# Kernel tuning notes

Measured on AMD Instinct MI355X. Metric: run time of the kernel, lower is better.

Reference implementation:

```python
import jax, jax.numpy as jnp
import numpy as np

B, N, D, H, L = 2, 1024, 256, 4, 18
HD = D // H  # 64 per-head dim
SINKHORN_ITERS = 100
EPS = 1e-6


def _ln(x, g, b):
    # repo's custom LayerNorm: normalize over channel dim (-2) of [B,C,N], torch.std is unbiased (ddof=1)
    mean = jnp.mean(x, axis=1, keepdims=True)
    std = jnp.std(x, axis=1, keepdims=True, ddof=1)
    return g[None, :, None] * (x - mean) / (std + EPS) + b[None, :, None]


def _conv(w, b, x):
    # Conv1d kernel_size=1 on [B,Cin,N] == pointwise linear
    return jnp.einsum('oi,bin->bon', w, x) + b[None, :, None]


def setup_inputs() -> dict:
    key = jax.random.key(0)
    ks = iter(jax.random.split(key, 64))
    def nrm(shape, scale=1.0):
        return jax.random.normal(next(ks), shape, dtype=jnp.float32) * scale
    inp = {}
    inp['desc0'] = nrm((B, D, N))
    inp['desc1'] = nrm((B, D, N))
    inp['kpts0'] = jax.random.uniform(next(ks), (B, N, 2), dtype=jnp.float32)
    inp['kpts1'] = jax.random.uniform(next(ks), (B, N, 2), dtype=jnp.float32)
    inp['scores0'] = jax.random.uniform(next(ks), (B, N), dtype=jnp.float32)
    inp['scores1'] = jax.random.uniform(next(ks), (B, N), dtype=jnp.float32)
    ch = [3, 32, 64, 128, 256]
    for i in range(4):
        ci, co = ch[i], ch[i + 1]
        inp['kenc_w%d' % i] = nrm((co, ci), 1.0 / np.sqrt(ci))
        inp['kenc_b%d' % i] = jnp.zeros((co,), jnp.float32)
        if i < 3:
            inp['kenc_g%d' % i] = jnp.ones((co,), jnp.float32)
            inp['kenc_be%d' % i] = jnp.zeros((co,), jnp.float32)
    s = 1.0 / np.sqrt(D)
    for nm in ['q', 'k', 'v', 'm']:
        inp['gnn_%sw' % nm] = nrm((L, D, D), s)
        inp['gnn_%sb' % nm] = jnp.zeros((L, D), jnp.float32)
    inp['gnn_w1'] = nrm((L, 2 * D, 2 * D), 1.0 / np.sqrt(2 * D))
    inp['gnn_b1'] = jnp.zeros((L, 2 * D), jnp.float32)
    inp['gnn_g1'] = jnp.ones((L, 2 * D), jnp.float32)
    inp['gnn_be1'] = jnp.zeros((L, 2 * D), jnp.float32)
    inp['gnn_w2'] = nrm((L, D, 2 * D), 1.0 / np.sqrt(2 * D))
    inp['gnn_b2'] = jnp.zeros((L, D), jnp.float32)
    inp['final_w'] = nrm((D, D), s)
    inp['final_b'] = jnp.zeros((D,), jnp.float32)
    return inp


def reference(desc0, desc1, kpts0, kpts1, scores0, scores1, kenc_w0, kenc_b0, kenc_g0, kenc_be0, kenc_w1, kenc_b1, kenc_g1, kenc_be1, kenc_w2, kenc_b2, kenc_g2, kenc_be2, kenc_w3, kenc_b3, gnn_qw, gnn_qb, gnn_kw, gnn_kb, gnn_vw, gnn_vb, gnn_mw, gnn_mb, gnn_w1, gnn_b1, gnn_g1, gnn_be1, gnn_w2, gnn_b2, final_w, final_b):
    def kenc(kpts, sc):
        x = jnp.concatenate([jnp.transpose(kpts, (0, 2, 1)), sc[:, None, :]], axis=1)  # [B,3,N]
        x = jax.nn.relu(_ln(_conv(kenc_w0, kenc_b0, x), kenc_g0, kenc_be0))
        x = jax.nn.relu(_ln(_conv(kenc_w1, kenc_b1, x), kenc_g1, kenc_be1))
        x = jax.nn.relu(_ln(_conv(kenc_w2, kenc_b2, x), kenc_g2, kenc_be2))
        return _conv(kenc_w3, kenc_b3, x)

    d0 = desc0 + kenc(kpts0, scores0)
    d1 = desc1 + kenc(kpts1, scores1)

    def gnn_layer(i, x, src):
        b = x.shape[0]
        q = _conv(gnn_qw[i], gnn_qb[i], x).reshape(b, HD, H, -1)
        k = _conv(gnn_kw[i], gnn_kb[i], src).reshape(b, HD, H, -1)
        v = _conv(gnn_vw[i], gnn_vb[i], src).reshape(b, HD, H, -1)
        sc = jnp.einsum('bdhn,bdhm->bhnm', q, k) / np.sqrt(HD).astype(np.float32)
        prob = jax.nn.softmax(sc, axis=-1)
        msg = jnp.einsum('bhnm,bdhm->bdhn', prob, v).reshape(b, D, -1)
        msg = _conv(gnn_mw[i], gnn_mb[i], msg)
        y = jnp.concatenate([x, msg], axis=1)  # [B,2D,N]
        y = jax.nn.relu(_ln(_conv(gnn_w1[i], gnn_b1[i], y), gnn_g1[i], gnn_be1[i]))
        return _conv(gnn_w2[i], gnn_b2[i], y)

    for i in range(L):  # names alternate self(even)/cross(odd)
        if i % 2 == 1:
            s0, s1 = d1, d0
        else:
            s0, s1 = d0, d1
        d0n = d0 + gnn_layer(i, d0, s0)
        d1n = d1 + gnn_layer(i, d1, s1)
        d0, d1 = d0n, d1n

    m0 = _conv(final_w, final_b, d0)
    m1 = _conv(final_w, final_b, d1)
    sc = jnp.einsum('bdn,bdm->bnm', m0, m1) / np.sqrt(D).astype(np.float32)

    # log-domain Sinkhorn with uniform marginals log_mu = log_nu = -log(m+n)
    n = sc.shape[1]
    norm = -jnp.log(jnp.asarray(2.0 * n, dtype=sc.dtype))
    u0 = jnp.zeros(sc.shape[:2], sc.dtype)
    v0 = jnp.zeros(sc.shape[:2], sc.dtype)

    def body(_, uv):
        u, v = uv
        u = norm - jax.scipy.special.logsumexp(sc + v[:, None, :], axis=2)
        v = norm - jax.scipy.special.logsumexp(sc + u[:, :, None], axis=1)
        return (u, v)

    u, v = jax.lax.fori_loop(0, SINKHORN_ITERS, body, (u0, v0))
    Z = sc + u[:, :, None] + v[:, None, :] - norm
    return Z
```

## Files before the change

### kernel.cpp

```cpp
#include <hip/hip_runtime.h>


#define NPOS 1024
#define DIM  256
#define NLAYER 18

static constexpr float NORMC = -7.6246189861593985f;

typedef float f32x4 __attribute__((ext_vector_type(4)));
typedef unsigned int u32x2 __attribute__((ext_vector_type(2)));
typedef unsigned int u32x4 __attribute__((ext_vector_type(4)));

__device__ __forceinline__ float wredmax(float v){
#pragma unroll
  for (int o = 32; o > 0; o >>= 1) v = fmaxf(v, __shfl_xor(v, o));
  return v;
}
__device__ __forceinline__ float wredsum(float v){
#pragma unroll
  for (int o = 32; o > 0; o >>= 1) v += __shfl_xor(v, o);
  return v;
}

__device__ __forceinline__ void cvt2(float x, unsigned short& h, unsigned short& l){
  unsigned xb = __float_as_uint(x);
  h = (unsigned short)(xb >> 16);
  float r = x - __uint_as_float(xb & 0xFFFF0000u);
  l = (unsigned short)(__float_as_uint(r) >> 16);
}
__device__ __forceinline__ u32x2 pack4(const unsigned short* s){
  u32x2 p;
  p.x = (unsigned)s[0] | ((unsigned)s[1] << 16);
  p.y = (unsigned)s[2] | ((unsigned)s[3] << 16);
  return p;
}
__device__ __forceinline__ void mfma_bf16(f32x4& acc, const u32x4& a, const u32x4& b){
  asm volatile("v_mfma_f32_16x16x32_bf16 %0, %1, %2, %0" : "+v"(acc) : "v"(a), "v"(b));
}
__device__ __forceinline__ void mfma_bf16_hz(f32x4& acc, const u32x4& a, const u32x4& b){
  asm volatile("s_nop 3\n\tv_mfma_f32_16x16x32_bf16 %0, %1, %2, %0" : "+v"(acc) : "v"(a), "v"(b));
}
#define MFMA_FENCE() asm volatile("s_nop 7\n\ts_nop 7\n\ts_nop 7" :::)


template<bool RESID, bool SPLIT>
__device__ __forceinline__ void gemm_mfma_core(
    const float* __restrict__ W, const float* __restrict__ bias,
    const float* __restrict__ Xb, const float* __restrict__ X2b,
    float* __restrict__ Ob, const float* __restrict__ Rb,
    int K, int o0, int n0)
{
  __shared__ unsigned short lwh[4096], lwl[4096];
  __shared__ unsigned short lxh[4096], lxl[4096];
  const int t = threadIdx.x;
  const int lane = t & 63, w = t >> 6;
  f32x4 acc[4];
#pragma unroll
  for (int i = 0; i < 4; i++) acc[i] = (f32x4)0.f;

  const int so = t & 63, skq = (t >> 6) << 4;
  const int sn = t & 63, skg = t >> 6;
  const int wmi = so >> 4, wol = so & 15;
  const int wks = skq >> 5, whalf = (skq >> 4) & 1;
  const int xni = sn >> 4, xnl = sn & 15;
  const int xks = skg >> 1, xhalf = skg & 1;

  float4 pw[4];
  float px[16];
  const float* wbase = W + (long)(o0 + so) * K + skq;
  auto loadchunk = [&](int kp) {
#pragma unroll
    for (int q = 0; q < 4; q++) pw[q] = *(const float4*)(wbase + kp + q * 4);
    const float* xr = (SPLIT && kp >= 256) ? (X2b + (long)(kp - 256) * NPOS)
                                           : (Xb + (long)kp * NPOS);
#pragma unroll
    for (int q = 0; q < 4; q++)
#pragma unroll
      for (int j = 0; j < 4; j++)
        px[q * 4 + j] = xr[(long)(skg * 16 + q * 4 + j) * NPOS + n0 + sn];
  };

  loadchunk(0);
  for (int kp = 0; kp < K; kp += 64) {
#pragma unroll
    for (int q = 0; q < 4; q++) {
      unsigned short h[4], l[4];
      cvt2(pw[q].x, h[0], l[0]); cvt2(pw[q].y, h[1], l[1]);
      cvt2(pw[q].z, h[2], l[2]); cvt2(pw[q].w, h[3], l[3]);
      int idx = ((wmi * 2 + wks) * 64 + wol + 16 * q) * 8 + whalf * 4;
      *(u32x2*)&lwh[idx] = pack4(h);
      *(u32x2*)&lwl[idx] = pack4(l);
    }
#pragma unroll
    for (int q = 0; q < 4; q++) {
      unsigned short h[4], l[4];
#pragma unroll
      for (int j = 0; j < 4; j++) cvt2(px[q * 4 + j], h[j], l[j]);
      int idx = ((xni * 2 + xks) * 64 + xnl + 16 * q) * 8 + xhalf * 4;
      *(u32x2*)&lxh[idx] = pack4(h);
      *(u32x2*)&lxl[idx] = pack4(l);
    }
    __syncthreads();
    if (kp + 64 < K) loadchunk(kp + 64);
#pragma unroll
    for (int ks = 0; ks < 2; ks++) {
      u32x4 Bh = *(const u32x4*)&lxh[((w * 2 + ks) * 64 + lane) * 8];
      u32x4 Bl = *(const u32x4*)&lxl[((w * 2 + ks) * 64 + lane) * 8];
#pragma unroll
      for (int mi = 0; mi < 4; mi++) {
        u32x4 Ah = *(const u32x4*)&lwh[((mi * 2 + ks) * 64 + lane) * 8];
        u32x4 Al = *(const u32x4*)&lwl[((mi * 2 + ks) * 64 + lane) * 8];
        mfma_bf16(acc[mi], Ah, Bh);
        mfma_bf16(acc[mi], Ah, Bl);
        mfma_bf16(acc[mi], Al, Bh);
      }
    }
    __syncthreads();
  }
  MFMA_FENCE();
  const int l15 = lane & 15, l4 = lane >> 4;
  const int n = n0 + (w << 4) + l15;
#pragma unroll
  for (int mi = 0; mi < 4; mi++) {
#pragma unroll
    for (int r = 0; r < 4; r++) {
      int o = o0 + mi * 16 + l4 * 4 + r;
      float val = acc[mi][r] + bias[o];
      if (RESID) val += Rb[(long)o * NPOS + n];
      Ob[(long)o * NPOS + n] = val;
    }
  }
}

template<bool RESID, bool SPLIT>
__global__ __launch_bounds__(256, 4) void gemm_mfma(
    const float* __restrict__ W, const float* __restrict__ bias,
    const float* __restrict__ X, const float* __restrict__ X2,
    float* __restrict__ out, const float* __restrict__ R,
    int K, long xbs, long x2bs, long obs, long rbs)
{
  const int bz = blockIdx.z;
  gemm_mfma_core<RESID, SPLIT>(W, bias,
      X + (long)bz * xbs, SPLIT ? (X2 + (long)bz * x2bs) : X,
      out + (long)bz * obs, RESID ? (R + (long)bz * rbs) : out,
      K, blockIdx.y * 64, blockIdx.x * 64);
}

__global__ __launch_bounds__(256, 4) void gemm_qkv_mfma(
    const float* __restrict__ Wq, const float* __restrict__ Bq,
    const float* __restrict__ Wk, const float* __restrict__ Bk,
    const float* __restrict__ Wv, const float* __restrict__ Bv,
    const float* __restrict__ X, float* __restrict__ out)
{
  const int z = blockIdx.z;
  const int which = z >> 2, bz = z & 3;
  const float* W    = (which == 0) ? Wq : (which == 1) ? Wk : Wv;
  const float* bias = (which == 0) ? Bq : (which == 1) ? Bk : Bv;
  gemm_mfma_core<false, false>(W, bias,
      X + (long)bz * (DIM * NPOS), nullptr,
      out + (long)which * 1048576 + (long)bz * (DIM * NPOS), nullptr,
      256, blockIdx.y * 64, blockIdx.x * 64);
}

__global__ __launch_bounds__(256, 4) void gemm_w1s_mfma(
    const float* __restrict__ W, const float* __restrict__ bias,
    const float* __restrict__ X, const float* __restrict__ X2,
    float* __restrict__ out, float* __restrict__ psum, float* __restrict__ psq)
{
  __shared__ unsigned short lwh[4096], lwl[4096];
  __shared__ unsigned short lxh[4096], lxl[4096];
  const int t = threadIdx.x;
  const int lane = t & 63, w = t >> 6;
  const int bz = blockIdx.z, o0 = blockIdx.y * 64, n0 = blockIdx.x * 64;
  const float* Xb  = X  + (long)bz * (DIM * NPOS);
  const float* X2b = X2 + (long)bz * (DIM * NPOS);
  float* Ob = out + (long)bz * (2L * DIM * NPOS);
  f32x4 acc[4];
#pragma unroll
  for (int i = 0; i < 4; i++) acc[i] = (f32x4)0.f;

  const int so = t & 63, skq = (t >> 6) << 4;
  const int sn = t & 63, skg = t >> 6;
  const int wmi = so >> 4, wol = so & 15;
  const int wks = skq >> 5, whalf = (skq >> 4) & 1;
  const int xni = sn >> 4, xnl = sn & 15;
  const int xks = skg >> 1, xhalf = skg & 1;

  float4 pw[4];
  float px[16];
  const float* wbase = W + (long)(o0 + so) * 512 + skq;
  auto loadchunk = [&](int kp) {
#pragma unroll
    for (int q = 0; q < 4; q++) pw[q] = *(const float4*)(wbase + kp + q * 4);
    const float* xr = (kp >= 256) ? (X2b + (long)(kp - 256) * NPOS)
                                  : (Xb + (long)kp * NPOS);
#pragma unroll
    for (int q = 0; q < 4; q++)
#pragma unroll
      for (int j = 0; j < 4; j++)
        px[q * 4 + j] = xr[(long)(skg * 16 + q * 4 + j) * NPOS + n0 + sn];
  };

  loadchunk(0);
  for (int kp = 0; kp < 512; kp += 64) {
#pragma unroll
    for (int q = 0; q < 4; q++) {
      unsigned short h[4], l[4];
      cvt2(pw[q].x, h[0], l[0]); cvt2(pw[q].y, h[1], l[1]);
      cvt2(pw[q].z, h[2], l[2]); cvt2(pw[q].w, h[3], l[3]);
      int idx = ((wmi * 2 + wks) * 64 + wol + 16 * q) * 8 + whalf * 4;
      *(u32x2*)&lwh[idx] = pack4(h);
      *(u32x2*)&lwl[idx] = pack4(l);
    }
#pragma unroll
    for (int q = 0; q < 4; q++) {
      unsigned short h[4], l[4];
#pragma unroll
      for (int j = 0; j < 4; j++) cvt2(px[q * 4 + j], h[j], l[j]);
      int idx = ((xni * 2 + xks) * 64 + xnl + 16 * q) * 8 + xhalf * 4;
      *(u32x2*)&lxh[idx] = pack4(h);
      *(u32x2*)&lxl[idx] = pack4(l);
    }
    __syncthreads();
    if (kp + 64 < 512) loadchunk(kp + 64);
#pragma unroll
    for (int ks = 0; ks < 2; ks++) {
      u32x4 Bh = *(const u32x4*)&lxh[((w * 2 + ks) * 64 + lane) * 8];
      u32x4 Bl = *(const u32x4*)&lxl[((w * 2 + ks) * 64 + lane) * 8];
#pragma unroll
      for (int mi = 0; mi < 4; mi++) {
        u32x4 Ah = *(const u32x4*)&lwh[((mi * 2 + ks) * 64 + lane) * 8];
        u32x4 Al = *(const u32x4*)&lwl[((mi * 2 + ks) * 64 + lane) * 8];
        mfma_bf16(acc[mi], Ah, Bh);
        mfma_bf16(acc[mi], Ah, Bl);
        mfma_bf16(acc[mi], Al, Bh);
      }
    }
    __syncthreads();
  }
  MFMA_FENCE();
  const int l15 = lane & 15, l4 = lane >> 4;
  const int n = n0 + (w << 4) + l15;
  float ps = 0.f, pq = 0.f;
#pragma unroll
  for (int mi = 0; mi < 4; mi++) {
#pragma unroll
    for (int r = 0; r < 4; r++) {
      int o = o0 + mi * 16 + l4 * 4 + r;
      float val = acc[mi][r] + bias[o];
      Ob[(long)o * NPOS + n] = val;
      ps += val; pq += val * val;
    }
  }
  ps += __shfl_xor(ps, 16); ps += __shfl_xor(ps, 32);
  pq += __shfl_xor(pq, 16); pq += __shfl_xor(pq, 32);
  if (l4 == 0) {
    long sidx = ((long)blockIdx.y * 4 + bz) * NPOS + n;
    psum[sidx] = ps;
    psq[sidx]  = pq;
  }
}

__global__ __launch_bounds__(256, 4) void gemm_w2ln_mfma(
    const float* __restrict__ W, const float* __restrict__ bias,
    const float* __restrict__ X, const float* __restrict__ ga, const float* __restrict__ be,
    const float* __restrict__ psum, const float* __restrict__ psq,
    float* __restrict__ out, const float* __restrict__ R)
{
  __shared__ unsigned short lwh[4096], lwl[4096];
  __shared__ unsigned short lxh[4096], lxl[4096];
  __shared__ float meanv[64], invv[64];
  const int t = threadIdx.x;
  const int lane = t & 63, w = t >> 6;
  const int bz = blockIdx.z, o0 = blockIdx.y * 64, n0 = blockIdx.x * 64;
  const float* Xb = X + (long)bz * (2L * DIM * NPOS);
  float* Ob = out + (long)bz * (DIM * NPOS);
  const float* Rb = R + (long)bz * (DIM * NPOS);
  if (t < 64) {
    int n = n0 + t;
    float S = 0.f, S2 = 0.f;
#pragma unroll
    for (int j = 0; j < 8; j++) {
      long sidx = ((long)j * 4 + bz) * NPOS + n;
      S += psum[sidx]; S2 += psq[sidx];
    }
    float mean = S * (1.f / 512.f);
    float var  = (S2 - 512.f * mean * mean) * (1.f / 511.f);
    meanv[t] = mean;
    invv[t]  = 1.f / (sqrtf(fmaxf(var, 0.f)) + 1e-6f);
  }
  __syncthreads();

  f32x4 acc[4];
#pragma unroll
  for (int i = 0; i < 4; i++) acc[i] = (f32x4)0.f;

  const int so = t & 63, skq = (t >> 6) << 4;
  const int sn = t & 63, skg = t >> 6;
  const int wmi = so >> 4, wol = so & 15;
  const int wks = skq >> 5, whalf = (skq >> 4) & 1;
  const int xni = sn >> 4, xnl = sn & 15;
  const int xks = skg >> 1, xhalf = skg & 1;
  const float mn = meanv[sn], iv = invv[sn];

  float4 pw[4];
  float px[16];
  const float* wbase = W + (long)(o0 + so) * 512 + skq;
  auto loadchunk = [&](int kp) {
#pragma unroll
    for (int q = 0; q < 4; q++) pw[q] = *(const float4*)(wbase + kp + q * 4);
#pragma unroll
    for (int q = 0; q < 4; q++)
#pragma unroll
      for (int j = 0; j < 4; j++)
        px[q * 4 + j] = Xb[(long)(kp + skg * 16 + q * 4 + j) * NPOS + n0 + sn];
  };

  loadchunk(0);
  for (int kp = 0; kp < 512; kp += 64) {
#pragma unroll
    for (int q = 0; q < 4; q++) {
      unsigned short h[4], l[4];
      cvt2(pw[q].x, h[0], l[0]); cvt2(pw[q].y, h[1], l[1]);
      cvt2(pw[q].z, h[2], l[2]); cvt2(pw[q].w, h[3], l[3]);
      int idx = ((wmi * 2 + wks) * 64 + wol + 16 * q) * 8 + whalf * 4;
      *(u32x2*)&lwh[idx] = pack4(h);
      *(u32x2*)&lwl[idx] = pack4(l);
    }
#pragma unroll
    for (int q = 0; q < 4; q++) {
      unsigned short h[4], l[4];
#pragma unroll
      for (int j = 0; j < 4; j++) {
        int cc = kp + skg * 16 + q * 4 + j;
        float x = fmaxf((px[q * 4 + j] - mn) * iv * ga[cc] + be[cc], 0.f);
        cvt2(x, h[j], l[j]);
      }
      int idx = ((xni * 2 + xks) * 64 + xnl + 16 * q) * 8 + xhalf * 4;
      *(u32x2*)&lxh[idx] = pack4(h);
      *(u32x2*)&lxl[idx] = pack4(l);
    }
    __syncthreads();
    if (kp + 64 < 512) loadchunk(kp + 64);
#pragma unroll
    for (int ks = 0; ks < 2; ks++) {
      u32x4 Bh = *(const u32x4*)&lxh[((w * 2 + ks) * 64 + lane) * 8];
      u32x4 Bl = *(const u32x4*)&lxl[((w * 2 + ks) * 64 + lane) * 8];
#pragma unroll
      for (int mi = 0; mi < 4; mi++) {
        u32x4 Ah = *(const u32x4*)&lwh[((mi * 2 + ks) * 64 + lane) * 8];
        u32x4 Al = *(const u32x4*)&lwl[((mi * 2 + ks) * 64 + lane) * 8];
        mfma_bf16(acc[mi], Ah, Bh);
        mfma_bf16(acc[mi], Ah, Bl);
        mfma_bf16(acc[mi], Al, Bh);
      }
    }
    __syncthreads();
  }
  MFMA_FENCE();
  const int l15 = lane & 15, l4 = lane >> 4;
  const int n = n0 + (w << 4) + l15;
#pragma unroll
  for (int mi = 0; mi < 4; mi++) {
#pragma unroll
    for (int r = 0; r < 4; r++) {
      int o = o0 + mi * 16 + l4 * 4 + r;
      Ob[(long)o * NPOS + n] = acc[mi][r] + bias[o] + Rb[(long)o * NPOS + n];
    }
  }
}

__global__ __launch_bounds__(256) void scores_mfma(
    const float* __restrict__ Mm, float* __restrict__ S0, float* __restrict__ S1, float scale)
{
  __shared__ unsigned short lah[4096], lal[4096];
  __shared__ unsigned short lbh[8192], lbl[8192];
  const int t = threadIdx.x, lane = t & 63, w = t >> 6;
  const int m0 = blockIdx.x * 128, n0 = blockIdx.y * 64;
  const int g = blockIdx.z & 1, dir = blockIdx.z >> 1;
  const long BS2 = 2L * DIM * NPOS;
  const float* Ag = (dir ? (Mm + BS2) : Mm) + (long)g * DIM * NPOS;
  const float* Bg = (dir ? Mm : (Mm + BS2)) + (long)g * DIM * NPOS;
  float* Sg = (dir ? S1 : S0) + (long)g * NPOS * NPOS;
  f32x4 acc[4][2];
#pragma unroll
  for (int i = 0; i < 4; i++)
#pragma unroll
    for (int j = 0; j < 2; j++) acc[i][j] = (f32x4)0.f;

  const int an = t & 63, acq = t >> 6;
  const int bm = t & 127, bkg = t >> 7;
  const int ami = an >> 4, anl = an & 15;
  const int aks = acq >> 1, ahalf = acq & 1;
  const int bni = bm >> 4, bnl = bm & 15;

  for (int cp = 0; cp < 256; cp += 64) {
#pragma unroll
    for (int q = 0; q < 4; q++) {
      unsigned short h[4], l[4];
#pragma unroll
      for (int j = 0; j < 4; j++) {
        float x = Ag[(long)(cp + acq * 16 + q * 4 + j) * NPOS + n0 + an];
        cvt2(x, h[j], l[j]);
      }
      int idx = ((ami * 2 + aks) * 64 + anl + 16 * q) * 8 + ahalf * 4;
      *(u32x2*)&lah[idx] = pack4(h);
      *(u32x2*)&lal[idx] = pack4(l);
    }
#pragma unroll
    for (int q = 0; q < 8; q++) {
      unsigned short h[4], l[4];
#pragma unroll
      for (int j = 0; j < 4; j++) {
        float x = Bg[(long)(cp + bkg * 32 + q * 4 + j) * NPOS + m0 + bm];
        cvt2(x, h[j], l[j]);
      }
      int qm = q & 3, half = (q >> 2) & 1;
      int idx = ((bni * 2 + bkg) * 64 + bnl + 16 * qm) * 8 + half * 4;
      *(u32x2*)&lbh[idx] = pack4(h);
      *(u32x2*)&lbl[idx] = pack4(l);
    }
    __syncthreads();
#pragma unroll
    for (int ks = 0; ks < 2; ks++) {
      u32x4 Ah[4], Al[4], Bh[2], Bl[2];
#pragma unroll
      for (int mi = 0; mi < 4; mi++) {
        Ah[mi] = *(const u32x4*)&lah[((mi * 2 + ks) * 64 + lane) * 8];
        Al[mi] = *(const u32x4*)&lal[((mi * 2 + ks) * 64 + lane) * 8];
      }
#pragma unroll
      for (int ni = 0; ni < 2; ni++) {
        int gg = w * 2 + ni;
        Bh[ni] = *(const u32x4*)&lbh[((gg * 2 + ks) * 64 + lane) * 8];
        Bl[ni] = *(const u32x4*)&lbl[((gg * 2 + ks) * 64 + lane) * 8];
      }
#pragma unroll
      for (int mi = 0; mi < 4; mi++)
#pragma unroll
        for (int ni = 0; ni < 2; ni++) {
          mfma_bf16(acc[mi][ni], Ah[mi], Bh[ni]);
          mfma_bf16(acc[mi][ni], Ah[mi], Bl[ni]);
          mfma_bf16(acc[mi][ni], Al[mi], Bh[ni]);
        }
    }
    __syncthreads();
  }
  MFMA_FENCE();
  const int l15 = lane & 15, l4 = lane >> 4;
#pragma unroll
  for (int mi = 0; mi < 4; mi++)
#pragma unroll
    for (int r = 0; r < 4; r++) {
      int n = n0 + mi * 16 + l4 * 4 + r;
#pragma unroll
      for (int ni = 0; ni < 2; ni++) {
        int m = m0 + (w * 2 + ni) * 16 + l15;
        Sg[(long)n * NPOS + m] = acc[mi][ni][r] * scale;
      }
    }
}

__global__ __launch_bounds__(256) void flash_mfma(
    const float* __restrict__ Q, const float* __restrict__ K,
    const float* __restrict__ V, float* __restrict__ O, int cross)
{
  __shared__ unsigned short lqh[4096], lql[4096];
  __shared__ unsigned short lkh[4096], lkl[4096];
  __shared__ unsigned short lvh[4096], lvl[4096];
  const int t = threadIdx.x, lane = t & 63, w = t >> 6;
  const int lin = blockIdx.x + 16 * blockIdx.y;
  const int xcd = lin & 7, slot = lin >> 3;
  const int g = xcd * 2 + (slot >> 4);
  const int n0 = (slot & 15) * 64;
  const int s = g >> 3, b = (g >> 2) & 1, h = g & 3;
  const int sba = s * 2 + b;
  const int sbb = (cross ? (1 - s) : s) * 2 + b;
  const float* Qg = Q + ((long)sba * DIM + h) * NPOS;
  const float* Kg = K + ((long)sbb * DIM + h) * NPOS;
  const float* Vg = V + ((long)sbb * DIM + h) * NPOS;
  float*       Og = O + ((long)sba * DIM + h) * NPOS;

  {
    const int n = t & 63;
#pragma unroll
    for (int qq = 0; qq < 4; qq++) {
      int dq = (t >> 6) + qq * 4;
      unsigned short hh[4], ll[4];
#pragma unroll
      for (int j = 0; j < 4; j++) {
        float x = Qg[(long)(4 * (dq * 4 + j)) * NPOS + n0 + n] * 0.125f;
        cvt2(x, hh[j], ll[j]);
      }
      int idx = (((n >> 4) * 2 + (dq >> 3)) * 64 + (n & 15) + 16 * (dq & 3)) * 8 + ((dq >> 2) & 1) * 4;
      *(u32x2*)&lqh[idx] = pack4(hh);
      *(u32x2*)&lql[idx] = pack4(ll);
    }
  }

  float M = -1e30f, L = 0.f;
  f32x4 acc_o[4];
#pragma unroll
  for (int i = 0; i < 4; i++) acc_o[i] = (f32x4)0.f;

  const int km = t & 63;
  const int vmq = t & 15;
  float pk[16];
  float4 pv4[4];
  auto loadKV = [&](int m0) {
#pragma unroll
    for (int qq = 0; qq < 4; qq++) {
      int dq = (t >> 6) + qq * 4;
#pragma unroll
      for (int j = 0; j < 4; j++)
        pk[qq * 4 + j] = Kg[(long)(4 * (dq * 4 + j)) * NPOS + m0 + km];
    }
#pragma unroll
    for (int pp = 0; pp < 4; pp++) {
      int d = (t >> 4) + pp * 16;
      pv4[pp] = *(const float4*)(Vg + (long)(4 * d) * NPOS + m0 + vmq * 4);
    }
  };

  loadKV(0);
  for (int mt = 0; mt < 16; mt++) {
    __syncthreads();
#pragma unroll
    for (int qq = 0; qq < 4; qq++) {
      int dq = (t >> 6) + qq * 4;
      unsigned short hh[4], ll[4];
#pragma unroll
      for (int j = 0; j < 4; j++) cvt2(pk[qq * 4 + j], hh[j], ll[j]);
      int idx = (((km >> 4) * 2 + (dq >> 3)) * 64 + (km & 15) + 16 * (dq & 3)) * 8 + ((dq >> 2) & 1) * 4;
      *(u32x2*)&lkh[idx] = pack4(hh);
      *(u32x2*)&lkl[idx] = pack4(ll);
    }
#pragma unroll
    for (int pp = 0; pp < 4; pp++) {
      int d = (t >> 4) + pp * 16;
      unsigned short hh[4], ll[4];
      cvt2(pv4[pp].x, hh[0], ll[0]); cvt2(pv4[pp].y, hh[1], ll[1]);
      cvt2(pv4[pp].z, hh[2], ll[2]); cvt2(pv4[pp].w, hh[3], ll[3]);
      int idx = (((d >> 4) * 2 + (vmq >> 3)) * 64 + (d & 15) + 16 * (vmq & 3)) * 8 + ((vmq >> 2) & 1) * 4;
      *(u32x2*)&lvh[idx] = pack4(hh);
      *(u32x2*)&lvl[idx] = pack4(ll);
    }
    __syncthreads();
    if (mt + 1 < 16) loadKV((mt + 1) * 64);

    f32x4 s_[4];
#pragma unroll
    for (int ms = 0; ms < 4; ms++) s_[ms] = (f32x4)0.f;
#pragma unroll
    for (int ks = 0; ks < 2; ks++) {
      u32x4 Bh = *(const u32x4*)&lqh[((w * 2 + ks) * 64 + lane) * 8];
      u32x4 Bl = *(const u32x4*)&lql[((w * 2 + ks) * 64 + lane) * 8];
#pragma unroll
      for (int ms = 0; ms < 4; ms++) {
        u32x4 Ah = *(const u32x4*)&lkh[((ms * 2 + ks) * 64 + lane) * 8];
        u32x4 Al = *(const u32x4*)&lkl[((ms * 2 + ks) * 64 + lane) * 8];
        mfma_bf16_hz(s_[ms], Ah, Bh);
        mfma_bf16_hz(s_[ms], Ah, Bl);
        mfma_bf16_hz(s_[ms], Al, Bh);
      }
    }
    MFMA_FENCE();

    float p[4][4];
    float tm = -1e30f;
#pragma unroll
    for (int ms = 0; ms < 4; ms++)
#pragma unroll
      for (int r = 0; r < 4; r++) tm = fmaxf(tm, s_[ms][r]);
    tm = fmaxf(tm, __shfl_xor(tm, 16));
    tm = fmaxf(tm, __shfl_xor(tm, 32));
    float nm = fmaxf(M, tm);
    float fi = __expf(M - nm);
    float rs = 0.f;
#pragma unroll
    for (int ms = 0; ms < 4; ms++)
#pragma unroll
      for (int r = 0; r < 4; r++) {
        float pv = __expf(s_[ms][r] - nm);
        p[ms][r] = pv; rs += pv;
      }
    rs += __shfl_xor(rs, 16);
    rs += __shfl_xor(rs, 32);
    L = L * fi + rs;
    M = nm;

    u32x4 Bp_h[2], Bp_l[2];
#pragma unroll
    for (int ks = 0; ks < 2; ks++) {
      unsigned short h0[4], l0[4], h1[4], l1[4];
#pragma unroll
      for (int r = 0; r < 4; r++) {
        cvt2(p[2 * ks][r], h0[r], l0[r]);
        cvt2(p[2 * ks + 1][r], h1[r], l1[r]);
      }
      u32x2 a = pack4(h0), bq = pack4(h1);
      Bp_h[ks].x = a.x; Bp_h[ks].y = a.y; Bp_h[ks].z = bq.x; Bp_h[ks].w = bq.y;
      u32x2 c = pack4(l0), dq = pack4(l1);
      Bp_l[ks].x = c.x; Bp_l[ks].y = c.y; Bp_l[ks].z = dq.x; Bp_l[ks].w = dq.y;
    }
#pragma unroll
    for (int ds = 0; ds < 4; ds++)
#pragma unroll
      for (int r = 0; r < 4; r++) acc_o[ds][r] *= fi;

#pragma unroll
    for (int ks = 0; ks < 2; ks++)
#pragma unroll
      for (int ds = 0; ds < 4; ds++) {
        u32x4 Ah = *(const u32x4*)&lvh[((ds * 2 + ks) * 64 + lane) * 8];
        u32x4 Al = *(const u32x4*)&lvl[((ds * 2 + ks) * 64 + lane) * 8];
        mfma_bf16_hz(acc_o[ds], Ah, Bp_h[ks]);
        mfma_bf16_hz(acc_o[ds], Ah, Bp_l[ks]);
        mfma_bf16_hz(acc_o[ds], Al, Bp_h[ks]);
      }
    MFMA_FENCE();
  }

  MFMA_FENCE();
  float linv = 1.f / L;
  const int nn = n0 + (w << 4) + (lane & 15);
#pragma unroll
  for (int ds = 0; ds < 4; ds++)
#pragma unroll
    for (int r = 0; r < 4; r++) {
      int d = ds * 16 + (lane >> 4) * 4 + r;
      Og[(long)(4 * d) * NPOS + nn] = acc_o[ds][r] * linv;
    }
}

__global__ __launch_bounds__(256) void foldW1(
    const float* __restrict__ w1g, const float* __restrict__ mwg,
    const float* __restrict__ b1g, const float* __restrict__ mbg,
    float* __restrict__ Wcat, float* __restrict__ bcat)
{
  const int z = blockIdx.z;
  const float* W1 = w1g + (long)z * 262144;
  const float* Wm = mwg + (long)z * 65536;
  float* out = Wcat + (long)z * 262144;
  const int o0 = blockIdx.y * 64;
  const int t = threadIdx.x;
  if (blockIdx.x >= 4) {
    const int c0 = (int)(blockIdx.x - 4) * 64;
    const int row = t >> 2, cb = (t & 3) * 16;
#pragma unroll
    for (int q = 0; q < 4; q++) {
      *(float4*)(out + (long)(o0 + row) * 512 + c0 + cb + 4 * q) =
          *(const float4*)(W1 + (long)(o0 + row) * 512 + c0 + cb + 4 * q);
    }
    if (blockIdx.x == 4 && t < 64) {
      int o = o0 + t;
      float acc = b1g[z * 512 + o];
      const float* wr = W1 + (long)o * 512 + 256;
      const float* bm = mbg + z * 256;
      for (int j = 0; j < 256; j++) acc += wr[j] * bm[j];
      bcat[z * 512 + o] = acc;
    }
    return;
  }
  __shared__ float As[16][64], Xs[16][64];
  const int c0 = blockIdx.x * 64;
  const int lr = t >> 2, lc = (t & 3) << 2;
  const int xr = t >> 4, xc = (t & 15) << 2;
  const int ty = t >> 4, tx = t & 15;
  float acc[4][4] = {};
  for (int j0 = 0; j0 < 256; j0 += 16) {
    float4 av = *(const float4*)(W1 + (long)(o0 + lr) * 512 + 256 + j0 + lc);
    As[lc + 0][lr] = av.x; As[lc + 1][lr] = av.y; As[lc + 2][lr] = av.z; As[lc + 3][lr] = av.w;
    *(float4*)&Xs[xr][xc] = *(const float4*)(Wm + (long)(j0 + xr) * 256 + c0 + xc);
    __syncthreads();
#pragma unroll
    for (int kk = 0; kk < 16; kk++) {
      float4 a4 = *(const float4*)&As[kk][ty << 2];
      float4 b4 = *(const float4*)&Xs[kk][tx << 2];
      acc[0][0] += a4.x * b4.x; acc[0][1] += a4.x * b4.y; acc[0][2] += a4.x * b4.z; acc[0][3] += a4.x * b4.w;
      acc[1][0] += a4.y * b4.x; acc[1][1] += a4.y * b4.y; acc[1][2] += a4.y * b4.z; acc[1][3] += a4.y * b4.w;
      acc[2][0] += a4.z * b4.x; acc[2][1] += a4.z * b4.y; acc[2][2] += a4.z * b4.z; acc[2][3] += a4.z * b4.w;
      acc[3][0] += a4.w * b4.x; acc[3][1] += a4.w * b4.y; acc[3][2] += a4.w * b4.z; acc[3][3] += a4.w * b4.w;
    }
    __syncthreads();
  }
#pragma unroll
  for (int i = 0; i < 4; i++) {
    float4 v = make_float4(acc[i][0], acc[i][1], acc[i][2], acc[i][3]);
    *(float4*)(out + (long)(o0 + (ty << 2) + i) * 512 + 256 + c0 + (tx << 2)) = v;
  }
}

__global__ __launch_bounds__(256) void sinkK(const float* __restrict__ S,
                                             const float* __restrict__ vin,
                                             float* __restrict__ uout, float norm)
{
  const int r = blockIdx.x * 4 + (threadIdx.x >> 6);
  const int lane = threadIdx.x & 63;
  const int b = r >> 10;
  const float* row = S + (long)r * NPOS;
  const float* vv = vin + (b << 10);
  float vals[16]; float mx = -1e30f;
#pragma unroll
  for (int i = 0; i < 16; i++) { vals[i] = row[lane + i * 64] + vv[lane + i * 64]; mx = fmaxf(mx, vals[i]); }
  mx = wredmax(mx);
  float s = 0.f;
#pragma unroll
  for (int i = 0; i < 16; i++) s += __expf(vals[i] - mx);
  s = wredsum(s);
  if (lane == 0) uout[r] = norm - (mx + __logf(s));
}

__global__ __launch_bounds__(256) void finZ(float* __restrict__ Z, const float* __restrict__ u,
                                            const float* __restrict__ v, float norm)
{
  long i = (long)blockIdx.x * 256 + threadIdx.x;
  float4 z = ((float4*)Z)[i];
  long e = i << 2;
  int b = (int)(e >> 20); int n = (int)((e >> 10) & 1023); int m = (int)(e & 1023);
  float add = u[(b << 10) + n] - norm;
  const float* vb = v + (b << 10) + m;
  z.x += add + vb[0]; z.y += add + vb[1]; z.z += add + vb[2]; z.w += add + vb[3];
  ((float4*)Z)[i] = z;
}

template<int O, int I>
__device__ __forceinline__ void stage_mm(const float* __restrict__ W, const float* __restrict__ bias,
                                         const float* xin, float* xout, int g, int p)
{
  for (int o = g; o < O; o += 4) {
    float acc = bias[o];
    const float* wr = W + o * I;
    for (int i = 0; i < I; i++) acc += wr[i] * xin[i * 64 + p];
    xout[o * 64 + p] = acc;
  }
  __syncthreads();
}
template<int C>
__device__ __forceinline__ void stage_ln(float* x, const float* __restrict__ ga,
                                         const float* __restrict__ be, float* red, int g, int p)
{
  float s = 0.f, s2 = 0.f;
  for (int c = g; c < C; c += 4) { float v = x[c * 64 + p]; s += v; s2 += v * v; }
  red[g * 64 + p] = s; red[(4 + g) * 64 + p] = s2;
  __syncthreads();
  float S  = red[p] + red[64 + p] + red[128 + p] + red[192 + p];
  float S2 = red[256 + p] + red[320 + p] + red[384 + p] + red[448 + p];
  float mean = S / (float)C;
  float var  = (S2 - (float)C * mean * mean) / (float)(C - 1);
  float inv  = 1.f / (sqrtf(fmaxf(var, 0.f)) + 1e-6f);
  __syncthreads();
  for (int c = g; c < C; c += 4) {
    float v = (x[c * 64 + p] - mean) * inv * ga[c] + be[c];
    x[c * 64 + p] = fmaxf(v, 0.f);
  }
  __syncthreads();
}

__global__ __launch_bounds__(256) void kencK(
    const float* __restrict__ kpts0, const float* __restrict__ scr0, const float* __restrict__ desc0,
    const float* __restrict__ kpts1, const float* __restrict__ scr1, const float* __restrict__ desc1,
    const float* __restrict__ w0, const float* __restrict__ b0, const float* __restrict__ g0, const float* __restrict__ be0,
    const float* __restrict__ w1, const float* __restrict__ b1, const float* __restrict__ g1, const float* __restrict__ be1,
    const float* __restrict__ w2, const float* __restrict__ b2, const float* __restrict__ g2, const float* __restrict__ be2,
    const float* __restrict__ w3, const float* __restrict__ b3,
    float* __restrict__ dout)
{
  __shared__ float a0[3 * 64], a1[32 * 64], a2[64 * 64], a3[128 * 64], red[8 * 64];
  const int t = threadIdx.x, p = t & 63, g = t >> 6;
  const int strm = blockIdx.x >> 5;
  const int blk = blockIdx.x & 31;
  const float* kpts = strm ? kpts1 : kpts0;
  const float* scr  = strm ? scr1  : scr0;
  const float* desc = strm ? desc1 : desc0;
  float* dst = dout + (long)strm * 2 * DIM * NPOS;
  const int b = blk >> 4, n0 = (blk & 15) << 6;
  if (g == 0)      a0[p]        = kpts[((b << 10) + n0 + p) * 2];
  else if (g == 1) a0[64 + p]   = kpts[((b << 10) + n0 + p) * 2 + 1];
  else if (g == 2) a0[128 + p]  = scr[(b << 10) + n0 + p];
  __syncthreads();
  stage_mm<32, 3>(w0, b0, a0, a1, g, p);   stage_ln<32>(a1, g0, be0, red, g, p);
  stage_mm<64, 32>(w1, b1, a1, a2, g, p);  stage_ln<64>(a2, g1, be1, red, g, p);
  stage_mm<128, 64>(w2, b2, a2, a3, g, p); stage_ln<128>(a3, g2, be2, red, g, p);
  for (int o = g; o < 256; o += 4) {
    float acc = b3[o];
    const float* wr = w3 + o * 128;
    for (int i = 0; i < 128; i++) acc += wr[i] * a3[i * 64 + p];
    long idx = ((long)(b * 256 + o) << 10) + n0 + p;
    dst[idx] = desc[idx] + acc;
  }
}

extern "C" void kernel_launch(void* const* d_in, const int* in_sizes, int n_in,
                              void* d_out, int out_size, void* d_ws, size_t ws_size,
                              hipStream_t stream)
{
  (void)in_sizes; (void)n_in; (void)out_size; (void)ws_size;
  const float* desc0   = (const float*)d_in[0];
  const float* desc1   = (const float*)d_in[1];
  const float* kpts0   = (const float*)d_in[2];
  const float* kpts1   = (const float*)d_in[3];
  const float* scores0 = (const float*)d_in[4];
  const float* scores1 = (const float*)d_in[5];
  const float* kw0 = (const float*)d_in[6],  *kb0 = (const float*)d_in[7],
             * kg0 = (const float*)d_in[8],  *kbe0 = (const float*)d_in[9];
  const float* kw1 = (const float*)d_in[10], *kb1 = (const float*)d_in[11],
             * kg1 = (const float*)d_in[12], *kbe1 = (const float*)d_in[13];
  const float* kw2 = (const float*)d_in[14], *kb2 = (const float*)d_in[15],
             * kg2 = (const float*)d_in[16], *kbe2 = (const float*)d_in[17];
  const float* kw3 = (const float*)d_in[18], *kb3 = (const float*)d_in[19];
  const float* qw = (const float*)d_in[20], *qbi = (const float*)d_in[21];
  const float* kw = (const float*)d_in[22], *kbi = (const float*)d_in[23];
  const float* vw = (const float*)d_in[24], *vbi = (const float*)d_in[25];
  const float* mw = (const float*)d_in[26], *mbi = (const float*)d_in[27];
  const float* w1g = (const float*)d_in[28], *b1g = (const float*)d_in[29];
  const float* g1g = (const float*)d_in[30], *be1g = (const float*)d_in[31];
  const float* w2g = (const float*)d_in[32], *b2g = (const float*)d_in[33];
  const float* fw = (const float*)d_in[34], *fb = (const float*)d_in[35];

  float* ws = (float*)d_ws;
  const long M1 = 1048576;
  float* d_a  = ws;
  float* d_b  = ws + 1 * M1;
  float* qb   = ws + 2 * M1;
  float* kb   = ws + 3 * M1;
  float* vb   = ws + 4 * M1;
  float* msgb = ws + 5 * M1;
  float* Pb   = ws + 8 * M1;
  float* t1   = Pb;
  float* Wcat = ws + 10 * M1;
  float* bcat = ws + 15 * M1;
  float* psum = ws + 15 * M1 + 16384;
  float* psq  = psum + 32768;
  float* uu   = ws + 16 * M1;
  float* vv   = uu + 2048;
  float* scT  = qb;
  float* mmb  = msgb;

  foldW1<<<dim3(8, 8, 18), 256, 0, stream>>>(w1g, mw, b1g, mbi, Wcat, bcat);

  kencK<<<64, 256, 0, stream>>>(kpts0, scores0, desc0, kpts1, scores1, desc1,
      kw0, kb0, kg0, kbe0, kw1, kb1, kg1, kbe1, kw2, kb2, kg2, kbe2, kw3, kb3, d_a);

  float* dc = d_a; float* dn = d_b;
  const long BS1 = (long)DIM * NPOS;
  for (int i = 0; i < NLAYER; i++) {
    int cross = i & 1;
    const float* Wq = qw + (long)i * 65536;  const float* Bq = qbi + (long)i * 256;
    const float* Wk = kw + (long)i * 65536;  const float* Bk = kbi + (long)i * 256;
    const float* Wv = vw + (long)i * 65536;  const float* Bv = vbi + (long)i * 256;
    const float* W1 = Wcat + (long)i * 262144; const float* B1 = bcat + (long)i * 512;
    const float* G1 = g1g + (long)i * 512;    const float* BE1 = be1g + (long)i * 512;
    const float* W2 = w2g + (long)i * 131072; const float* B2 = b2g + (long)i * 256;

    gemm_qkv_mfma<<<dim3(16, 4, 12), 256, 0, stream>>>(Wq, Bq, Wk, Bk, Wv, Bv, dc, qb);
    flash_mfma<<<dim3(16, 16), 256, 0, stream>>>(qb, kb, vb, msgb, cross);
    gemm_w1s_mfma<<<dim3(16, 8, 4), 256, 0, stream>>>(W1, B1, dc, msgb, t1, psum, psq);
    gemm_w2ln_mfma<<<dim3(16, 4, 4), 256, 0, stream>>>(W2, B2, t1, G1, BE1, psum, psq, dn, dc);
    float* tmp = dc; dc = dn; dn = tmp;
  }

  gemm_mfma<false, false><<<dim3(16, 4, 4), 256, 0, stream>>>(
      fw, fb, dc, nullptr, mmb, nullptr, 256, BS1, 0, BS1, 0);
  float* scf = (float*)d_out;
  scores_mfma<<<dim3(8, 16, 4), 256, 0, stream>>>(mmb, scf, scT, 0.0625f);

  hipMemsetAsync(vv, 0, 2048 * sizeof(float), stream);
  for (int it = 0; it < 100; it++) {
    sinkK<<<512, 256, 0, stream>>>(scf, vv, uu, NORMC);
    sinkK<<<512, 256, 0, stream>>>(scT, uu, vv, NORMC);
  }
  finZ<<<2048, 256, 0, stream>>>(scf, uu, vv, NORMC);
}
```

Before: 2.387 ms.

## Split flash attention over key range with separate combine kernel

The attention kernel now splits the 1024 keys into two halves along a new grid dimension, doubling the block count from 256 to 512. Each block writes unnormalized partial outputs plus its running max and sum, and a new combine kernel merges the two halves with log-sum-exp rescaling. The aim is better occupancy of the GPU's compute units, since 256 blocks underfill the device. The cost is an extra kernel launch per layer and extra global traffic for the partial outputs.

```diff
diff --git a/kernel.cpp b/kernel.cpp
--- a/kernel.cpp
+++ b/kernel.cpp
@@ -461,15 +461,17 @@
     }
 }
 
-__global__ __launch_bounds__(256) void flash_mfma(
+__global__ __launch_bounds__(256) void flash_part(
     const float* __restrict__ Q, const float* __restrict__ K,
-    const float* __restrict__ V, float* __restrict__ O, int cross)
+    const float* __restrict__ V, float* __restrict__ Op,
+    float* __restrict__ Mp, float* __restrict__ Lp, int cross)
 {
   __shared__ unsigned short lqh[4096], lql[4096];
   __shared__ unsigned short lkh[4096], lkl[4096];
   __shared__ unsigned short lvh[4096], lvl[4096];
   const int t = threadIdx.x, lane = t & 63, w = t >> 6;
   const int lin = blockIdx.x + 16 * blockIdx.y;
+  const int split = blockIdx.z;
   const int xcd = lin & 7, slot = lin >> 3;
   const int g = xcd * 2 + (slot >> 4);
   const int n0 = (slot & 15) * 64;
@@ -479,7 +481,7 @@
   const float* Qg = Q + ((long)sba * DIM + h) * NPOS;
   const float* Kg = K + ((long)sbb * DIM + h) * NPOS;
   const float* Vg = V + ((long)sbb * DIM + h) * NPOS;
-  float*       Og = O + ((long)sba * DIM + h) * NPOS;
+  float*       Og = Op + (long)split * 1048576 + ((long)sba * DIM + h) * NPOS;
 
   {
     const int n = t & 63;
@@ -522,8 +524,9 @@
     }
   };
 
-  loadKV(0);
-  for (int mt = 0; mt < 16; mt++) {
+  const int mbase = split * 8;
+  loadKV(mbase * 64);
+  for (int mt = 0; mt < 8; mt++) {
     __syncthreads();
 #pragma unroll
     for (int qq = 0; qq < 4; qq++) {
@@ -546,7 +549,7 @@
       *(u32x2*)&lvl[idx] = pack4(ll);
     }
     __syncthreads();
-    if (mt + 1 < 16) loadKV((mt + 1) * 64);
+    if (mt + 1 < 8) loadKV((mbase + mt + 1) * 64);
 
     f32x4 s_[4];
 #pragma unroll
@@ -622,15 +625,55 @@
   }
 
   MFMA_FENCE();
-  float linv = 1.f / L;
   const int nn = n0 + (w << 4) + (lane & 15);
 #pragma unroll
   for (int ds = 0; ds < 4; ds++)
 #pragma unroll
     for (int r = 0; r < 4; r++) {
       int d = ds * 16 + (lane >> 4) * 4 + r;
-      Og[(long)(4 * d) * NPOS + nn] = acc_o[ds][r] * linv;
-    }
+      Og[(long)(4 * d) * NPOS + nn] = acc_o[ds][r];
+    }
+  if ((lane >> 4) == 0) {
+    Mp[(long)split * 16384 + g * 1024 + nn] = M;
+    Lp[(long)split * 16384 + g * 1024 + nn] = L;
+  }
+}
+
+__global__ __launch_bounds__(256) void combineK(
+    const float* __restrict__ Op, const float* __restrict__ Mp,
+    const float* __restrict__ Lp, float* __restrict__ O)
+{
+  long i = (long)blockIdx.x * 256 + threadIdx.x;
+  long e = i << 2;
+  int sb  = (int)(e >> 18);
+  int rem = (int)(e & 262143);
+  int row = rem >> 10, n = rem & 1023;
+  int h = row & 3;
+  int g = ((sb >> 1) << 3) + ((sb & 1) << 2) + h;
+  float4 oa = *(const float4*)(Op + e);
+  float4 ob = *(const float4*)(Op + 1048576 + e);
+  float4 ma = *(const float4*)(Mp + g * 1024 + n);
+  float4 mb = *(const float4*)(Mp + 16384 + g * 1024 + n);
+  float4 la = *(const float4*)(Lp + g * 1024 + n);
+  float4 lb = *(const float4*)(Lp + 16384 + g * 1024 + n);
+  float4 r;
+  {
+    float m = fmaxf(ma.x, mb.x); float ea = __expf(ma.x - m), eb = __expf(mb.x - m);
+    r.x = (oa.x * ea + ob.x * eb) / (la.x * ea + lb.x * eb);
+  }
+  {
+    float m = fmaxf(ma.y, mb.y); float ea = __expf(ma.y - m), eb = __expf(mb.y - m);
+    r.y = (oa.y * ea + ob.y * eb) / (la.y * ea + lb.y * eb);
+  }
+  {
+    float m = fmaxf(ma.z, mb.z); float ea = __expf(ma.z - m), eb = __expf(mb.z - m);
+    r.z = (oa.z * ea + ob.z * eb) / (la.z * ea + lb.z * eb);
+  }
+  {
+    float m = fmaxf(ma.w, mb.w); float ea = __expf(ma.w - m), eb = __expf(mb.w - m);
+    r.w = (oa.w * ea + ob.w * eb) / (la.w * ea + lb.w * eb);
+  }
+  *(float4*)(O + e) = r;
 }
 
 __global__ __launch_bounds__(256) void foldW1(
@@ -826,12 +869,15 @@
   float* kb   = ws + 3 * M1;
   float* vb   = ws + 4 * M1;
   float* msgb = ws + 5 * M1;
+  float* Opart = ws + 6 * M1;
   float* Pb   = ws + 8 * M1;
   float* t1   = Pb;
   float* Wcat = ws + 10 * M1;
   float* bcat = ws + 15 * M1;
   float* psum = ws + 15 * M1 + 16384;
   float* psq  = psum + 32768;
+  float* Mpart = psq + 32768;
+  float* Lpart = Mpart + 32768;
   float* uu   = ws + 16 * M1;
   float* vv   = uu + 2048;
   float* scT  = qb;
@@ -854,7 +900,8 @@
     const float* W2 = w2g + (long)i * 131072; const float* B2 = b2g + (long)i * 256;
 
     gemm_qkv_mfma<<<dim3(16, 4, 12), 256, 0, stream>>>(Wq, Bq, Wk, Bk, Wv, Bv, dc, qb);
-    flash_mfma<<<dim3(16, 16), 256, 0, stream>>>(qb, kb, vb, msgb, cross);
+    flash_part<<<dim3(16, 16, 2), 256, 0, stream>>>(qb, kb, vb, Opart, Mpart, Lpart, cross);
+    combineK<<<1024, 256, 0, stream>>>(Opart, Mpart, Lpart, msgb);
     gemm_w1s_mfma<<<dim3(16, 8, 4), 256, 0, stream>>>(W1, B1, dc, msgb, t1, psum, psq);
     gemm_w2ln_mfma<<<dim3(16, 4, 4), 256, 0, stream>>>(W2, B2, t1, G1, BE1, psum, psq, dn, dc);
     float* tmp = dc; dc = dn; dn = tmp;
```

After: 2.242 ms. -6.1%, faster.
